# Performance work log

Measured on AMD Instinct MI355X. Metric: run time of the kernel, lower is better.

Reference implementation:

```python
import jax, jax.numpy as jnp
import numpy as np


def _ln(x, g, b, eps=1e-5):
    m = jnp.mean(x, axis=-1, keepdims=True)
    v = jnp.mean((x - m) ** 2, axis=-1, keepdims=True)
    return (x - m) * jax.lax.rsqrt(v + eps) * g + b


def _mlp2(x, w1, b1, w2, b2):
    # Linear -> SiLU -> Linear
    return jax.nn.silu(x @ w1 + b1) @ w2 + b2


def setup_inputs() -> dict:
    key = jax.random.key(0)
    ks = jax.random.split(key, 32)
    B, H, W = 1, 128, 256
    N = H * W                  # 32768 nodes
    K = 6
    E = N * K                  # 196608 edges
    Cin, Cout = 70, 69
    D, De, Hd, L = 256, 128, 512, 8
    s = 0.02

    def rn(k, shape):
        return jax.random.normal(k, shape, jnp.float32) * s

    inp = {
        "x": jax.random.normal(ks[0], (B, Cin, H, W), jnp.float32),
        "edge_index": jax.random.randint(ks[1], (2, E), 0, N, dtype=jnp.int32).astype(jnp.int64),
        "raw_edge_feat": jax.random.normal(ks[2], (E, 3), jnp.float32),
        # node encoder
        "enc_w1": rn(ks[3], (Cin, D)), "enc_b1": jnp.zeros((D,), jnp.float32),
        "enc_w2": rn(ks[4], (D, D)),   "enc_b2": jnp.zeros((D,), jnp.float32),
        # edge encoder
        "eenc_w1": rn(ks[5], (3, De)),  "eenc_b1": jnp.zeros((De,), jnp.float32),
        "eenc_w2": rn(ks[6], (De, De)), "eenc_b2": jnp.zeros((De,), jnp.float32),
        # processor (stacked over L layers)
        "pe_w1": rn(ks[7], (L, 2 * D + De, Hd)), "pe_b1": jnp.zeros((L, Hd), jnp.float32),
        "pe_w2": rn(ks[8], (L, Hd, De)),         "pe_b2": jnp.zeros((L, De), jnp.float32),
        "pe_g": jnp.ones((L, De), jnp.float32),  "pe_bt": jnp.zeros((L, De), jnp.float32),
        "pn_w1": rn(ks[9], (L, D + De, Hd)),     "pn_b1": jnp.zeros((L, Hd), jnp.float32),
        "pn_w2": rn(ks[10], (L, Hd, D)),         "pn_b2": jnp.zeros((L, D), jnp.float32),
        "pn_g": jnp.ones((L, D), jnp.float32),   "pn_bt": jnp.zeros((L, D), jnp.float32),
        # node decoder
        "dec_w1": rn(ks[11], (D, D)),   "dec_b1": jnp.zeros((D,), jnp.float32),
        "dec_w2": rn(ks[12], (D, Cout)), "dec_b2": jnp.zeros((Cout,), jnp.float32),
    }
    return inp


def reference(x, edge_index, raw_edge_feat,
              enc_w1, enc_b1, enc_w2, enc_b2,
              eenc_w1, eenc_b1, eenc_w2, eenc_b2,
              pe_w1, pe_b1, pe_w2, pe_b2, pe_g, pe_bt,
              pn_w1, pn_b1, pn_w2, pn_b2, pn_g, pn_bt,
              dec_w1, dec_b1, dec_w2, dec_b2):
    B, C, H, W = x.shape
    N = H * W
    src, dst = edge_index[0], edge_index[1]

    # encode: (B, N, Cin) -> (B, N, D)
    node = _mlp2(jnp.transpose(x.reshape(B, C, N), (0, 2, 1)), enc_w1, enc_b1, enc_w2, enc_b2)
    # edge encoder shared across batch, then broadcast to (B, E, De)
    edge = _mlp2(raw_edge_feat, eenc_w1, eenc_b1, eenc_w2, eenc_b2)
    edge = jnp.broadcast_to(edge[None], (B,) + edge.shape)

    def step(carry, p):
        node, edge = carry
        ew1, eb1, ew2, eb2, eg, ebt, nw1, nb1, nw2, nb2, ng, nbt = p
        # edge update: gather src/dst node feats, residual MLP + LayerNorm
        inp = jnp.concatenate([node[:, src], node[:, dst], edge], axis=-1)  # (B, E, 2D+De)
        edge = _ln(edge + _mlp2(inp, ew1, eb1, ew2, eb2), eg, ebt)
        # aggregate edges into destination nodes (scatter_add)
        agg = jax.vmap(lambda e: jax.ops.segment_sum(e, dst, num_segments=N))(edge)
        # node update: residual MLP + LayerNorm
        node = _ln(node + _mlp2(jnp.concatenate([node, agg], axis=-1), nw1, nb1, nw2, nb2), ng, nbt)
        return (node, edge), None

    (node, edge), _ = jax.lax.scan(
        step, (node, edge),
        (pe_w1, pe_b1, pe_w2, pe_b2, pe_g, pe_bt,
         pn_w1, pn_b1, pn_w2, pn_b2, pn_g, pn_bt))

    out = _mlp2(node, dec_w1, dec_b1, dec_w2, dec_b2)          # (B, N, Cout)
    return jnp.transpose(out, (0, 2, 1)).reshape(B, -1, H, W)   # (B, Cout, H, W)
```

## Files before the change

### kernel.cpp

```cpp
#include <hip/hip_runtime.h>


typedef __attribute__((ext_vector_type(8))) short bf16x8;
typedef __attribute__((ext_vector_type(4))) float f32x4;
typedef unsigned short u16;

#define NNODES 32768
#define NEDGES 196608

#define MFMA16(a, b, c) __builtin_amdgcn_mfma_f32_16x16x32_bf16((a), (b), (c), 0, 0, 0)

__device__ __forceinline__ u16 f2bf(float f) {
    unsigned u = __float_as_uint(f);
    unsigned r = (u + 0x7FFFu + ((u >> 16) & 1u)) >> 16;
    return (u16)r;
}
__device__ __forceinline__ float bf2f(u16 b) {
    return __uint_as_float(((unsigned)b) << 16);
}
__device__ __forceinline__ unsigned pack2(float a, float b) {
    return (unsigned)f2bf(a) | ((unsigned)f2bf(b) << 16);
}

__global__ void wtrans_kernel(const float* __restrict__ W, u16* __restrict__ WT,
                              int K, int Nout, int Kpad, int NP) {
    __shared__ u16 tile[32][33];
    const int k0 = blockIdx.x * 32, n0 = blockIdx.y * 32;
    const int tx = threadIdx.x & 31, ty = threadIdx.x >> 5;
    #pragma unroll
    for (int i = 0; i < 4; i++) {
        int k = k0 + ty + 8 * i, n = n0 + tx;
        float v = (k < K && n < Nout) ? W[(size_t)k * Nout + n] : 0.f;
        tile[ty + 8 * i][tx] = f2bf(v);
    }
    __syncthreads();
    #pragma unroll
    for (int i = 0; i < 4; i++) {
        int n = n0 + ty + 8 * i, k = k0 + tx;
        if (n < NP && k < Kpad) WT[(size_t)n * Kpad + k] = tile[tx][ty + 8 * i];
    }
}

__global__ void fragpack_kernel(const float* __restrict__ W, u16* __restrict__ F,
                                int K, int N, int CB, int NFRAG) {
    int b = blockIdx.z;
    int fr = blockIdx.x * 4 + (threadIdx.x >> 6);
    if (fr >= NFRAG) return;
    int l = threadIdx.x & 63;
    int ks = fr / CB, cb = fr % CB;
    int k0 = ks * 32 + ((l >> 4) * 8);
    int n = cb * 16 + (l & 15);
    u16 v[8];
    #pragma unroll
    for (int j = 0; j < 8; j++) {
        int k = k0 + j;
        float x = (k < K && n < N) ? W[((size_t)b * K + k) * N + n] : 0.f;
        v[j] = f2bf(x);
    }
    *(uint4*)(F + (((size_t)b * NFRAG + fr) * 64 + l) * 8) = *(const uint4*)v;
}

__global__ void idx_norm_kernel(const int* __restrict__ raw, int* __restrict__ sd) {
    __shared__ int nz;
    if (threadIdx.x == 0) nz = 0;
    __syncthreads();
    for (int i = threadIdx.x; i < 512; i += 256)
        if (raw[2 * i + 1] != 0) atomicAdd(&nz, 1);
    __syncthreads();
    const bool is64 = (nz == 0);
    int idx = blockIdx.x * 256 + threadIdx.x;
    if (idx < 2 * NEDGES) sd[idx] = is64 ? raw[2 * idx] : raw[idx];
}

__global__ void csr_count_kernel(const int* __restrict__ dsti, int* __restrict__ deg) {
    int e = blockIdx.x * 256 + threadIdx.x;
    atomicAdd(&deg[dsti[e]], 1);
}

__global__ void csr_scan_kernel(const int* __restrict__ deg, int* __restrict__ off,
                                int* __restrict__ cur) {
    __shared__ int part[1024];
    const int t = threadIdx.x;
    int local[32];
    int s = 0;
    #pragma unroll
    for (int i = 0; i < 32; i++) { local[i] = deg[t * 32 + i]; s += local[i]; }
    part[t] = s;
    __syncthreads();
    for (int d = 1; d < 1024; d <<= 1) {
        int v = (t >= d) ? part[t - d] : 0;
        __syncthreads();
        part[t] += v;
        __syncthreads();
    }
    int excl = (t == 0) ? 0 : part[t - 1];
    #pragma unroll
    for (int i = 0; i < 32; i++) {
        off[t * 32 + i] = excl;
        cur[t * 32 + i] = excl;
        excl += local[i];
    }
    if (t == 1023) off[NNODES] = excl;
}

__global__ void csr_fill_kernel(const int* __restrict__ dsti, int* __restrict__ cur,
                                int* __restrict__ perm) {
    int e = blockIdx.x * 256 + threadIdx.x;
    int pos = atomicAdd(&cur[dsti[e]], 1);
    perm[pos] = e;
}

__global__ void gather_kernel(const u16* __restrict__ edge_b, const int* __restrict__ perm,
                              const int* __restrict__ off, u16* __restrict__ aggB) {
    int idx = blockIdx.x * 256 + threadIdx.x;
    int n = idx >> 5, c = (idx & 31) * 4;
    int a = off[n], b = off[n + 1];
    float s0 = 0.f, s1 = 0.f, s2 = 0.f, s3 = 0.f;
    for (int i = a; i < b; i++) {
        uint2 v = *(const uint2*)(edge_b + (size_t)perm[i] * 128 + c);
        s0 += bf2f((u16)(v.x & 0xffff)); s1 += bf2f((u16)(v.x >> 16));
        s2 += bf2f((u16)(v.y & 0xffff)); s3 += bf2f((u16)(v.y >> 16));
    }
    uint2 o;
    o.x = pack2(s0, s1);
    o.y = pack2(s2, s3);
    *(uint2*)(aggB + (size_t)n * 128 + c) = o;
}

struct MlpP {
    const u16* A1;
    const u16* A1b;
    const float* Araw;
    const int* src;
    const int* dsti;
    const u16* W1F;
    const u16* W2F;
    const float* b1;
    const float* b2;
    const float* g;
    const float* bt;
    const float* resid;
    float* outF;
    u16* outB;
    float* outDec;
};

template <int K1, int NH, int NOUT, int IN, int OUT, int A1S>
__global__ __launch_bounds__(256, 2) void mlp_kernel(MlpP p) {
    static_assert(K1 % 32 == 0 && NH % 128 == 0, "dims");
    constexpr int KSTEPS = K1 / 32;
    constexpr int NT1 = NH / 64;
    constexpr int CB1 = NH / 16;
    constexpr int NFRAG2 = (NOUT + 15) / 16;
    constexpr int NT2 = (NFRAG2 + 3) / 4;
    constexpr int S2 = NH / 64;
    constexpr int SH2 = NH / 2 + 8;
    constexpr int SH_BYTES = 64 * SH2 * 2;
    constexpr int SMEM_I = (SH_BYTES > 8192 ? SH_BYTES : 8192);
    constexpr int SMEM = SMEM_I + 2560;

    __shared__ __align__(16) char smem[SMEM];
    u16* sA = (u16*)smem;
    u16* sH = (u16*)smem;
    float* sS1 = (float*)(smem + SMEM_I);
    float* sS2 = sS1 + 256;
    float* sMu = sS1 + 512;
    float* sRs = sS1 + 576;

    const int tid = threadIdx.x;
    const int wave = tid >> 6, lane = tid & 63;
    const int lhi = lane >> 4, llo = lane & 15;
    const int r0 = blockIdx.x * 64;
    const int key = (llo >> 1) & 3;

    const int sr = tid >> 2;
    const int sg = (tid & 3) ^ ((sr >> 1) & 3);
    int gsrc = 0, gdst = 0;
    if constexpr (IN == 0) { gsrc = p.src[r0 + sr]; gdst = p.dsti[r0 + sr]; }

    auto loadA = [&](int ks, uint4& d) {
        const int kb = ks * 32;
        if constexpr (IN == 0) {
            if (kb < 256)      d = *(const uint4*)(p.A1 + (size_t)gsrc * 256 + kb + sg * 8);
            else if (kb < 512) d = *(const uint4*)(p.A1 + (size_t)gdst * 256 + (kb - 256) + sg * 8);
            else               d = *(const uint4*)(p.A1b + (size_t)(r0 + sr) * 128 + (kb - 512) + sg * 8);
        } else if constexpr (IN == 1) {
            if (kb < 256) d = *(const uint4*)(p.A1 + (size_t)(r0 + sr) * 256 + kb + sg * 8);
            else          d = *(const uint4*)(p.A1b + (size_t)(r0 + sr) * 128 + (kb - 256) + sg * 8);
        } else if constexpr (IN == 2) {
            d = *(const uint4*)(p.A1 + (size_t)(r0 + sr) * A1S + kb + sg * 8);
        } else {
            uint4 v = {0u, 0u, 0u, 0u};
            if (sg == 0) {
                const float* q = p.Araw + (size_t)(r0 + sr) * 3;
                v.x = pack2(q[0], q[1]);
                v.y = pack2(q[2], 0.f);
            }
            d = v;
        }
    };
    auto loadB1 = [&](int ks, bf16x8 (&d)[NT1]) {
        #pragma unroll
        for (int j = 0; j < NT1; j++) {
            int cb = j * 4 + wave;
            d[j] = *(const bf16x8*)(p.W1F + ((size_t)(ks * CB1 + cb) * 64 + lane) * 8);
        }
    };

    const f32x4 fz = {0.f, 0.f, 0.f, 0.f};
    f32x4 acc[4][NT1];
    #pragma unroll
    for (int m = 0; m < 4; m++)
        #pragma unroll
        for (int j = 0; j < NT1; j++) acc[m][j] = fz;

    uint4 pa0, pa1, pa2;
    bf16x8 pb0[NT1], pb1[NT1];
    loadA(0, pa0);
    if constexpr (KSTEPS > 1) loadA(1, pa1);
    if constexpr (KSTEPS > 2) loadA(2, pa2);
    loadB1(0, pb0);
    if constexpr (KSTEPS > 1) loadB1(1, pb1);

    #pragma unroll
    for (int ks = 0; ks < KSTEPS; ks++) {
        uint4* sAw = (uint4*)(sA + (ks & 1) * 2048);
        sAw[tid] = (ks % 3 == 0) ? pa0 : (ks % 3 == 1) ? pa1 : pa2;
        if (ks + 3 < KSTEPS) {
            if (ks % 3 == 0) loadA(ks + 3, pa0);
            else if (ks % 3 == 1) loadA(ks + 3, pa1);
            else loadA(ks + 3, pa2);
        }
        __syncthreads();
        const u16* sAr = sA + (ks & 1) * 2048;
        bf16x8 a[4];
        #pragma unroll
        for (int m = 0; m < 4; m++)
            a[m] = *(const bf16x8*)(sAr + (m * 16 + llo) * 32 + (lhi ^ key) * 8);
        bf16x8 (&pbc)[NT1] = (ks & 1) ? pb1 : pb0;
        #pragma unroll
        for (int j = 0; j < NT1; j++)
            #pragma unroll
            for (int m = 0; m < 4; m++) acc[m][j] = MFMA16(a[m], pbc[j], acc[m][j]);
        if (ks + 2 < KSTEPS) loadB1(ks + 2, pbc);
    }
    __syncthreads();

    f32x4 acc2[4][NT2];
    #pragma unroll
    for (int m = 0; m < 4; m++)
        #pragma unroll
        for (int j = 0; j < NT2; j++) acc2[m][j] = fz;

    auto loadW2 = [&](int g, bf16x8 (&d)[NT2]) {
        #pragma unroll
        for (int j = 0; j < NT2; j++) {
            int f = j * 4 + wave;
            if (NFRAG2 % 4 == 0 || f < NFRAG2)
                d[j] = *(const bf16x8*)(p.W2F + ((size_t)(g * NFRAG2 + f) * 64 + lane) * 8);
        }
    };
    bf16x8 pw0[NT2], pw1[NT2];
    loadW2(0, pw0);
    loadW2(1, pw1);

    #pragma unroll
    for (int half = 0; half < 2; half++) {
        #pragma unroll
        for (int j = half * (NT1 / 2); j < (half + 1) * (NT1 / 2); j++) {
            int c = (j * 4 + wave) * 16 + llo;
            int coll = c - half * (NH / 2);
            float bias = p.b1[c];
            #pragma unroll
            for (int m = 0; m < 4; m++)
                #pragma unroll
                for (int r = 0; r < 4; r++) {
                    int row = m * 16 + lhi * 4 + r;
                    float v = acc[m][j][r] + bias;
                    float sgm = __builtin_amdgcn_rcpf(1.f + __expf(-v));
                    sH[row * SH2 + coll] = f2bf(v * sgm);
                }
        }
        __syncthreads();
        #pragma unroll
        for (int s = 0; s < S2; s++) {
            const int g = half * S2 + s;
            bf16x8 (&pwc)[NT2] = (g & 1) ? pw1 : pw0;
            bf16x8 a2[4];
            #pragma unroll
            for (int m = 0; m < 4; m++)
                a2[m] = *(const bf16x8*)(sH + (m * 16 + llo) * SH2 + s * 32 + lhi * 8);
            #pragma unroll
            for (int j = 0; j < NT2; j++)
                if (NFRAG2 % 4 == 0 || j * 4 + wave < NFRAG2)
                    #pragma unroll
                    for (int m = 0; m < 4; m++)
                        acc2[m][j] = MFMA16(a2[m], pwc[j], acc2[m][j]);
            if (g + 2 < 2 * S2) loadW2(g + 2, pwc);
        }
        __syncthreads();
    }

    if constexpr (OUT == 0) {
        float ps1[4][4], ps2[4][4];
        #pragma unroll
        for (int m = 0; m < 4; m++)
            #pragma unroll
            for (int r = 0; r < 4; r++) { ps1[m][r] = 0.f; ps2[m][r] = 0.f; }
        #pragma unroll
        for (int j = 0; j < NT2; j++) {
            int col = (j * 4 + wave) * 16 + llo;
            float bias = p.b2[col];
            #pragma unroll
            for (int m = 0; m < 4; m++)
                #pragma unroll
                for (int r = 0; r < 4; r++) {
                    int row = m * 16 + lhi * 4 + r;
                    float v = acc2[m][j][r] + bias + p.resid[(size_t)(r0 + row) * NOUT + col];
                    acc2[m][j][r] = v;
                    ps1[m][r] += v;
                    ps2[m][r] += v * v;
                }
        }
        #pragma unroll
        for (int mm = 1; mm < 16; mm <<= 1)
            #pragma unroll
            for (int m = 0; m < 4; m++)
                #pragma unroll
                for (int r = 0; r < 4; r++) {
                    ps1[m][r] += __shfl_xor(ps1[m][r], mm, 64);
                    ps2[m][r] += __shfl_xor(ps2[m][r], mm, 64);
                }
        if (llo == 0) {
            #pragma unroll
            for (int m = 0; m < 4; m++)
                #pragma unroll
                for (int r = 0; r < 4; r++) {
                    int row = m * 16 + lhi * 4 + r;
                    sS1[wave * 64 + row] = ps1[m][r];
                    sS2[wave * 64 + row] = ps2[m][r];
                }
        }
        __syncthreads();
        if (tid < 64) {
            float a = sS1[tid] + sS1[64 + tid] + sS1[128 + tid] + sS1[192 + tid];
            float b = sS2[tid] + sS2[64 + tid] + sS2[128 + tid] + sS2[192 + tid];
            float mu = a * (1.f / NOUT);
            float var = b * (1.f / NOUT) - mu * mu;
            sMu[tid] = mu;
            sRs[tid] = rsqrtf(var + 1e-5f);
        }
        __syncthreads();
        #pragma unroll
        for (int j = 0; j < NT2; j++) {
            int col = (j * 4 + wave) * 16 + llo;
            float gg = p.g[col], bb = p.bt[col];
            #pragma unroll
            for (int m = 0; m < 4; m++)
                #pragma unroll
                for (int r = 0; r < 4; r++) {
                    int row = m * 16 + lhi * 4 + r;
                    float v = (acc2[m][j][r] - sMu[row]) * sRs[row] * gg + bb;
                    size_t o = (size_t)(r0 + row) * NOUT + col;
                    p.outF[o] = v;
                    p.outB[o] = f2bf(v);
                }
        }
    } else if constexpr (OUT == 1) {
        #pragma unroll
        for (int j = 0; j < NT2; j++) {
            int col = (j * 4 + wave) * 16 + llo;
            float bias = p.b2[col];
            #pragma unroll
            for (int m = 0; m < 4; m++)
                #pragma unroll
                for (int r = 0; r < 4; r++) {
                    int row = m * 16 + lhi * 4 + r;
                    float v = acc2[m][j][r] + bias;
                    size_t o = (size_t)(r0 + row) * NOUT + col;
                    p.outF[o] = v;
                    p.outB[o] = f2bf(v);
                }
        }
    } else {
        #pragma unroll
        for (int j = 0; j < NT2; j++) {
            int f = j * 4 + wave;
            int col = f * 16 + llo;
            if (f < NFRAG2 && col < 69) {
                float bias = p.b2[col];
                #pragma unroll
                for (int m = 0; m < 4; m++)
                    #pragma unroll
                    for (int r = 0; r < 4; r++) {
                        int row = m * 16 + lhi * 4 + r;
                        p.outDec[(size_t)col * NNODES + (r0 + row)] = acc2[m][j][r] + bias;
                    }
            }
        }
    }
}

extern "C" void kernel_launch(void* const* d_in, const int* in_sizes, int n_in,
                              void* d_out, int out_size, void* d_ws, size_t ws_size,
                              hipStream_t stream) {
    (void)in_sizes; (void)n_in; (void)out_size; (void)ws_size;

    const float* x       = (const float*)d_in[0];
    const int*   eidx    = (const int*)d_in[1];
    const float* raw_e   = (const float*)d_in[2];
    const float* enc_w1  = (const float*)d_in[3];
    const float* enc_b1  = (const float*)d_in[4];
    const float* enc_w2  = (const float*)d_in[5];
    const float* enc_b2  = (const float*)d_in[6];
    const float* eenc_w1 = (const float*)d_in[7];
    const float* eenc_b1 = (const float*)d_in[8];
    const float* eenc_w2 = (const float*)d_in[9];
    const float* eenc_b2 = (const float*)d_in[10];
    const float* pe_w1   = (const float*)d_in[11];
    const float* pe_b1   = (const float*)d_in[12];
    const float* pe_w2   = (const float*)d_in[13];
    const float* pe_b2   = (const float*)d_in[14];
    const float* pe_g    = (const float*)d_in[15];
    const float* pe_bt   = (const float*)d_in[16];
    const float* pn_w1   = (const float*)d_in[17];
    const float* pn_b1   = (const float*)d_in[18];
    const float* pn_w2   = (const float*)d_in[19];
    const float* pn_b2   = (const float*)d_in[20];
    const float* pn_g    = (const float*)d_in[21];
    const float* pn_bt   = (const float*)d_in[22];
    const float* dec_w1  = (const float*)d_in[23];
    const float* dec_b1  = (const float*)d_in[24];
    const float* dec_w2  = (const float*)d_in[25];
    const float* dec_b2  = (const float*)d_in[26];

    char* ws = (char*)d_ws;
    size_t o = 0;
    auto alloc = [&](size_t bytes) -> void* {
        void* p = ws + o;
        o += (bytes + 255) & ~(size_t)255;
        return p;
    };
    float* node_f = (float*)alloc((size_t)NNODES * 256 * 4);
    u16*   node_b = (u16*)  alloc((size_t)NNODES * 256 * 2);
    float* edge_f = (float*)alloc((size_t)NEDGES * 128 * 4);
    u16*   edge_b = (u16*)  alloc((size_t)NEDGES * 128 * 2);
    u16*   aggB   = (u16*)  alloc((size_t)NNODES * 128 * 2);
    u16*   xT     = (u16*)  alloc((size_t)NNODES * 96 * 2);
    u16*   encw1F  = (u16*)alloc((size_t)96 * 256 * 2);
    u16*   encw2F  = (u16*)alloc((size_t)256 * 256 * 2);
    u16*   eencw1F = (u16*)alloc((size_t)32 * 128 * 2);
    u16*   eencw2F = (u16*)alloc((size_t)128 * 128 * 2);
    u16*   pew1F   = (u16*)alloc((size_t)8 * 640 * 512 * 2);
    u16*   pew2F   = (u16*)alloc((size_t)8 * 512 * 128 * 2);
    u16*   pnw1F   = (u16*)alloc((size_t)8 * 384 * 512 * 2);
    u16*   pnw2F   = (u16*)alloc((size_t)8 * 512 * 256 * 2);
    u16*   decw1F  = (u16*)alloc((size_t)256 * 256 * 2);
    u16*   decw2F  = (u16*)alloc((size_t)256 * 80 * 2);
    int*   sd     = (int*)  alloc((size_t)2 * NEDGES * 4);
    int*   deg    = (int*)  alloc((size_t)NNODES * 4);
    int*   off_   = (int*)  alloc((size_t)(NNODES + 1) * 4);
    int*   cur    = (int*)  alloc((size_t)NNODES * 4);
    int*   perm   = (int*)  alloc((size_t)NEDGES * 4);

    auto FP = [&](const float* W, u16* F, int K, int N, int KB, int CB, int batch) {
        int nf = KB * CB;
        dim3 g((nf + 3) / 4, 1, batch);
        fragpack_kernel<<<g, 256, 0, stream>>>(W, F, K, N, CB, nf);
    };
    FP(enc_w1,  encw1F,  70,  256, 3,  16, 1);
    FP(enc_w2,  encw2F,  256, 256, 8,  16, 1);
    FP(eenc_w1, eencw1F, 3,   128, 1,  8,  1);
    FP(eenc_w2, eencw2F, 128, 128, 4,  8,  1);
    FP(pe_w1,   pew1F,   640, 512, 20, 32, 8);
    FP(pe_w2,   pew2F,   512, 128, 16, 8,  8);
    FP(pn_w1,   pnw1F,   384, 512, 12, 32, 8);
    FP(pn_w2,   pnw2F,   512, 256, 16, 16, 8);
    FP(dec_w1,  decw1F,  256, 256, 8,  16, 1);
    FP(dec_w2,  decw2F,  256, 69,  8,  5,  1);
    {
        dim3 g(96 / 32, NNODES / 32, 1);
        wtrans_kernel<<<g, 256, 0, stream>>>(x, xT, 70, NNODES, 96, NNODES);
    }

    idx_norm_kernel<<<1536, 256, 0, stream>>>(eidx, sd);
    hipMemsetAsync(deg, 0, (size_t)NNODES * 4, stream);
    csr_count_kernel<<<NEDGES / 256, 256, 0, stream>>>(sd + NEDGES, deg);
    csr_scan_kernel<<<1, 1024, 0, stream>>>(deg, off_, cur);
    csr_fill_kernel<<<NEDGES / 256, 256, 0, stream>>>(sd + NEDGES, cur, perm);

    {
        MlpP p{};
        p.A1 = xT; p.W1F = encw1F; p.W2F = encw2F; p.b1 = enc_b1; p.b2 = enc_b2;
        p.outF = node_f; p.outB = node_b;
        mlp_kernel<96, 256, 256, 2, 1, 96><<<NNODES / 64, 256, 0, stream>>>(p);
    }
    {
        MlpP p{};
        p.Araw = raw_e; p.W1F = eencw1F; p.W2F = eencw2F; p.b1 = eenc_b1; p.b2 = eenc_b2;
        p.outF = edge_f; p.outB = edge_b;
        mlp_kernel<32, 128, 128, 3, 1, 0><<<NEDGES / 64, 256, 0, stream>>>(p);
    }

    for (int l = 0; l < 8; l++) {
        {
            MlpP p{};
            p.A1 = node_b; p.A1b = edge_b; p.src = sd; p.dsti = sd + NEDGES;
            p.W1F = pew1F + (size_t)l * 640 * 512;
            p.W2F = pew2F + (size_t)l * 512 * 128;
            p.b1 = pe_b1 + l * 512; p.b2 = pe_b2 + l * 128;
            p.g = pe_g + l * 128; p.bt = pe_bt + l * 128;
            p.resid = edge_f; p.outF = edge_f; p.outB = edge_b;
            mlp_kernel<640, 512, 128, 0, 0, 0><<<NEDGES / 64, 256, 0, stream>>>(p);
        }
        gather_kernel<<<NNODES * 32 / 256, 256, 0, stream>>>(edge_b, perm, off_, aggB);
        {
            MlpP p{};
            p.A1 = node_b; p.A1b = aggB;
            p.W1F = pnw1F + (size_t)l * 384 * 512;
            p.W2F = pnw2F + (size_t)l * 512 * 256;
            p.b1 = pn_b1 + l * 512; p.b2 = pn_b2 + l * 256;
            p.g = pn_g + l * 256; p.bt = pn_bt + l * 256;
            p.resid = node_f; p.outF = node_f; p.outB = node_b;
            mlp_kernel<384, 512, 256, 1, 0, 0><<<NNODES / 64, 256, 0, stream>>>(p);
        }
    }

    {
        MlpP p{};
        p.A1 = node_b; p.W1F = decw1F; p.W2F = decw2F; p.b1 = dec_b1; p.b2 = dec_b2;
        p.outDec = (float*)d_out;
        mlp_kernel<256, 256, 80, 2, 2, 256><<<NNODES / 64, 256, 0, stream>>>(p);
    }
}
```

Baseline: 2.265 ms.

## Store edges in dst-sorted order and load A fragments directly from global

Edges are permuted once into destination-sorted order: the edge encoder reads raw features through the permutation, and the per-layer edge MLP uses pre-sorted src/dst index arrays. The gather then reads contiguous edge rows without indirection. Separately, the first GEMM in the MLP kernel drops its LDS staging and barriers and loads A fragments straight from global memory into registers, prefetching one k-step ahead. This trades LDS traffic and syncs for uncoalesced 16-byte global loads and higher register pressure.

```diff
diff --git a/kernel.cpp b/kernel.cpp
--- a/kernel.cpp
+++ b/kernel.cpp
@@ -110,14 +110,22 @@
     perm[pos] = e;
 }
 
-__global__ void gather_kernel(const u16* __restrict__ edge_b, const int* __restrict__ perm,
+__global__ void esort_kernel(const int* __restrict__ sd, const int* __restrict__ perm,
+                             int* __restrict__ srcS, int* __restrict__ dstS) {
+    int i = blockIdx.x * 256 + threadIdx.x;
+    int e = perm[i];
+    srcS[i] = sd[e];
+    dstS[i] = sd[NEDGES + e];
+}
+
+__global__ void gather_kernel(const u16* __restrict__ edge_b,
                               const int* __restrict__ off, u16* __restrict__ aggB) {
     int idx = blockIdx.x * 256 + threadIdx.x;
     int n = idx >> 5, c = (idx & 31) * 4;
     int a = off[n], b = off[n + 1];
     float s0 = 0.f, s1 = 0.f, s2 = 0.f, s3 = 0.f;
     for (int i = a; i < b; i++) {
-        uint2 v = *(const uint2*)(edge_b + (size_t)perm[i] * 128 + c);
+        uint2 v = *(const uint2*)(edge_b + (size_t)i * 128 + c);
         s0 += bf2f((u16)(v.x & 0xffff)); s1 += bf2f((u16)(v.x >> 16));
         s2 += bf2f((u16)(v.y & 0xffff)); s3 += bf2f((u16)(v.y >> 16));
     }
@@ -155,12 +163,10 @@
     constexpr int NT2 = (NFRAG2 + 3) / 4;
     constexpr int S2 = NH / 64;
     constexpr int SH2 = NH / 2 + 8;
-    constexpr int SH_BYTES = 64 * SH2 * 2;
-    constexpr int SMEM_I = (SH_BYTES > 8192 ? SH_BYTES : 8192);
+    constexpr int SMEM_I = 64 * SH2 * 2;
     constexpr int SMEM = SMEM_I + 2560;
 
     __shared__ __align__(16) char smem[SMEM];
-    u16* sA = (u16*)smem;
     u16* sH = (u16*)smem;
     float* sS1 = (float*)(smem + SMEM_I);
     float* sS2 = sS1 + 256;
@@ -171,40 +177,65 @@
     const int wave = tid >> 6, lane = tid & 63;
     const int lhi = lane >> 4, llo = lane & 15;
     const int r0 = blockIdx.x * 64;
-    const int key = (llo >> 1) & 3;
-
-    const int sr = tid >> 2;
-    const int sg = (tid & 3) ^ ((sr >> 1) & 3);
-    int gsrc = 0, gdst = 0;
-    if constexpr (IN == 0) { gsrc = p.src[r0 + sr]; gdst = p.dsti[r0 + sr]; }
-
-    auto loadA = [&](int ks, uint4& d) {
+    const int ko = lhi * 8;
+
+    int rs[4], rd[4];
+    if constexpr (IN == 0) {
+        #pragma unroll
+        for (int m = 0; m < 4; m++) {
+            rs[m] = p.src[r0 + m * 16 + llo];
+            rd[m] = p.dsti[r0 + m * 16 + llo];
+        }
+    } else if constexpr (IN == 3) {
+        #pragma unroll
+        for (int m = 0; m < 4; m++) rs[m] = p.src[r0 + m * 16 + llo];
+    }
+
+    auto loadA4 = [&](int ks, bf16x8 (&d)[4]) {
         const int kb = ks * 32;
         if constexpr (IN == 0) {
-            if (kb < 256)      d = *(const uint4*)(p.A1 + (size_t)gsrc * 256 + kb + sg * 8);
-            else if (kb < 512) d = *(const uint4*)(p.A1 + (size_t)gdst * 256 + (kb - 256) + sg * 8);
-            else               d = *(const uint4*)(p.A1b + (size_t)(r0 + sr) * 128 + (kb - 512) + sg * 8);
+            if (kb < 256) {
+                #pragma unroll
+                for (int m = 0; m < 4; m++)
+                    d[m] = *(const bf16x8*)(p.A1 + (size_t)rs[m] * 256 + kb + ko);
+            } else if (kb < 512) {
+                #pragma unroll
+                for (int m = 0; m < 4; m++)
+                    d[m] = *(const bf16x8*)(p.A1 + (size_t)rd[m] * 256 + (kb - 256) + ko);
+            } else {
+                #pragma unroll
+                for (int m = 0; m < 4; m++)
+                    d[m] = *(const bf16x8*)(p.A1b + (size_t)(r0 + m * 16 + llo) * 128 + (kb - 512) + ko);
+            }
         } else if constexpr (IN == 1) {
-            if (kb < 256) d = *(const uint4*)(p.A1 + (size_t)(r0 + sr) * 256 + kb + sg * 8);
-            else          d = *(const uint4*)(p.A1b + (size_t)(r0 + sr) * 128 + (kb - 256) + sg * 8);
+            if (kb < 256) {
+                #pragma unroll
+                for (int m = 0; m < 4; m++)
+                    d[m] = *(const bf16x8*)(p.A1 + (size_t)(r0 + m * 16 + llo) * 256 + kb + ko);
+            } else {
+                #pragma unroll
+                for (int m = 0; m < 4; m++)
+                    d[m] = *(const bf16x8*)(p.A1b + (size_t)(r0 + m * 16 + llo) * 128 + (kb - 256) + ko);
+            }
         } else if constexpr (IN == 2) {
-            d = *(const uint4*)(p.A1 + (size_t)(r0 + sr) * A1S + kb + sg * 8);
+            #pragma unroll
+            for (int m = 0; m < 4; m++)
+                d[m] = *(const bf16x8*)(p.A1 + (size_t)(r0 + m * 16 + llo) * A1S + kb + ko);
         } else {
-            uint4 v = {0u, 0u, 0u, 0u};
-            if (sg == 0) {
-                const float* q = p.Araw + (size_t)(r0 + sr) * 3;
-                v.x = pack2(q[0], q[1]);
-                v.y = pack2(q[2], 0.f);
+            #pragma unroll
+            for (int m = 0; m < 4; m++) {
+                u16 v[8] = {0, 0, 0, 0, 0, 0, 0, 0};
+                if (lhi == 0) {
+                    const float* q = p.Araw + (size_t)rs[m] * 3;
+                    v[0] = f2bf(q[0]); v[1] = f2bf(q[1]); v[2] = f2bf(q[2]);
+                }
+                d[m] = *(const bf16x8*)v;
             }
-            d = v;
         }
     };
-    auto loadB1 = [&](int ks, bf16x8 (&d)[NT1]) {
-        #pragma unroll
-        for (int j = 0; j < NT1; j++) {
-            int cb = j * 4 + wave;
-            d[j] = *(const bf16x8*)(p.W1F + ((size_t)(ks * CB1 + cb) * 64 + lane) * 8);
-        }
+    auto loadB1frag = [&](int ks, int j) -> bf16x8 {
+        int cb = j * 4 + wave;
+        return *(const bf16x8*)(p.W1F + ((size_t)(ks * CB1 + cb) * 64 + lane) * 8);
     };
 
     const f32x4 fz = {0.f, 0.f, 0.f, 0.f};
@@ -214,37 +245,24 @@
         #pragma unroll
         for (int j = 0; j < NT1; j++) acc[m][j] = fz;
 
-    uint4 pa0, pa1, pa2;
-    bf16x8 pb0[NT1], pb1[NT1];
-    loadA(0, pa0);
-    if constexpr (KSTEPS > 1) loadA(1, pa1);
-    if constexpr (KSTEPS > 2) loadA(2, pa2);
-    loadB1(0, pb0);
-    if constexpr (KSTEPS > 1) loadB1(1, pb1);
+    bf16x8 paA[4], paB[4];
+    bf16x8 pb[NT1];
+    loadA4(0, paA);
+    #pragma unroll
+    for (int j = 0; j < NT1; j++) pb[j] = loadB1frag(0, j);
 
     #pragma unroll
     for (int ks = 0; ks < KSTEPS; ks++) {
-        uint4* sAw = (uint4*)(sA + (ks & 1) * 2048);
-        sAw[tid] = (ks % 3 == 0) ? pa0 : (ks % 3 == 1) ? pa1 : pa2;
-        if (ks + 3 < KSTEPS) {
-            if (ks % 3 == 0) loadA(ks + 3, pa0);
-            else if (ks % 3 == 1) loadA(ks + 3, pa1);
-            else loadA(ks + 3, pa2);
-        }
-        __syncthreads();
-        const u16* sAr = sA + (ks & 1) * 2048;
-        bf16x8 a[4];
-        #pragma unroll
-        for (int m = 0; m < 4; m++)
-            a[m] = *(const bf16x8*)(sAr + (m * 16 + llo) * 32 + (lhi ^ key) * 8);
-        bf16x8 (&pbc)[NT1] = (ks & 1) ? pb1 : pb0;
-        #pragma unroll
-        for (int j = 0; j < NT1; j++)
-            #pragma unroll
-            for (int m = 0; m < 4; m++) acc[m][j] = MFMA16(a[m], pbc[j], acc[m][j]);
-        if (ks + 2 < KSTEPS) loadB1(ks + 2, pbc);
-    }
-    __syncthreads();
+        bf16x8 (&cur)[4] = (ks & 1) ? paB : paA;
+        bf16x8 (&nxt)[4] = (ks & 1) ? paA : paB;
+        if (ks + 1 < KSTEPS) loadA4(ks + 1, nxt);
+        #pragma unroll
+        for (int j = 0; j < NT1; j++) {
+            #pragma unroll
+            for (int m = 0; m < 4; m++) acc[m][j] = MFMA16(cur[m], pb[j], acc[m][j]);
+            if (ks + 1 < KSTEPS) pb[j] = loadB1frag(ks + 1, j);
+        }
+    }
 
     f32x4 acc2[4][NT2];
     #pragma unroll
@@ -462,6 +480,8 @@
     int*   off_   = (int*)  alloc((size_t)(NNODES + 1) * 4);
     int*   cur    = (int*)  alloc((size_t)NNODES * 4);
     int*   perm   = (int*)  alloc((size_t)NEDGES * 4);
+    int*   srcS   = (int*)  alloc((size_t)NEDGES * 4);
+    int*   dstS   = (int*)  alloc((size_t)NEDGES * 4);
 
     auto FP = [&](const float* W, u16* F, int K, int N, int KB, int CB, int batch) {
         int nf = KB * CB;
@@ -488,6 +508,7 @@
     csr_count_kernel<<<NEDGES / 256, 256, 0, stream>>>(sd + NEDGES, deg);
     csr_scan_kernel<<<1, 1024, 0, stream>>>(deg, off_, cur);
     csr_fill_kernel<<<NEDGES / 256, 256, 0, stream>>>(sd + NEDGES, cur, perm);
+    esort_kernel<<<NEDGES / 256, 256, 0, stream>>>(sd, perm, srcS, dstS);
 
     {
         MlpP p{};
@@ -497,7 +518,8 @@
     }
     {
         MlpP p{};
-        p.Araw = raw_e; p.W1F = eencw1F; p.W2F = eencw2F; p.b1 = eenc_b1; p.b2 = eenc_b2;
+        p.Araw = raw_e; p.src = perm;
+        p.W1F = eencw1F; p.W2F = eencw2F; p.b1 = eenc_b1; p.b2 = eenc_b2;
         p.outF = edge_f; p.outB = edge_b;
         mlp_kernel<32, 128, 128, 3, 1, 0><<<NEDGES / 64, 256, 0, stream>>>(p);
     }
@@ -505,7 +527,7 @@
     for (int l = 0; l < 8; l++) {
         {
             MlpP p{};
-            p.A1 = node_b; p.A1b = edge_b; p.src = sd; p.dsti = sd + NEDGES;
+            p.A1 = node_b; p.A1b = edge_b; p.src = srcS; p.dsti = dstS;
             p.W1F = pew1F + (size_t)l * 640 * 512;
             p.W2F = pew2F + (size_t)l * 512 * 128;
             p.b1 = pe_b1 + l * 512; p.b2 = pe_b2 + l * 128;
@@ -513,7 +535,7 @@
             p.resid = edge_f; p.outF = edge_f; p.outB = edge_b;
             mlp_kernel<640, 512, 128, 0, 0, 0><<<NEDGES / 64, 256, 0, stream>>>(p);
         }
-        gather_kernel<<<NNODES * 32 / 256, 256, 0, stream>>>(edge_b, perm, off_, aggB);
+        gather_kernel<<<NNODES * 32 / 256, 256, 0, stream>>>(edge_b, off_, aggB);
         {
             MlpP p{};
             p.A1 = node_b; p.A1b = aggB;
```

Measured after the change: 3.613 ms. 1.6x slower.

## Store edges in destination-sorted order and drop fp32 residual copies

Applied to the files above, without the earlier changes.

Permutes edges into CSR (destination-sorted) order once up front, so the edge encoder reads raw features through perm and each layer's edge MLP uses sorted src/dst indices. The gather then reads contiguous edge rows instead of indirect rows through perm. The fp32 node and edge state buffers are also removed: residuals are read from and written to the bf16 copies only. This cuts memory traffic but lowers residual precision to bf16 across the 8 layers, which may reduce accuracy.

```diff
diff --git a/kernel.cpp b/kernel.cpp
--- a/kernel.cpp
+++ b/kernel.cpp
@@ -110,14 +110,22 @@
     perm[pos] = e;
 }
 
-__global__ void gather_kernel(const u16* __restrict__ edge_b, const int* __restrict__ perm,
+__global__ void esort_kernel(const int* __restrict__ sd, const int* __restrict__ perm,
+                             int* __restrict__ srcS, int* __restrict__ dstS) {
+    int i = blockIdx.x * 256 + threadIdx.x;
+    int e = perm[i];
+    srcS[i] = sd[e];
+    dstS[i] = sd[NEDGES + e];
+}
+
+__global__ void gather_kernel(const u16* __restrict__ edge_b,
                               const int* __restrict__ off, u16* __restrict__ aggB) {
     int idx = blockIdx.x * 256 + threadIdx.x;
     int n = idx >> 5, c = (idx & 31) * 4;
     int a = off[n], b = off[n + 1];
     float s0 = 0.f, s1 = 0.f, s2 = 0.f, s3 = 0.f;
     for (int i = a; i < b; i++) {
-        uint2 v = *(const uint2*)(edge_b + (size_t)perm[i] * 128 + c);
+        uint2 v = *(const uint2*)(edge_b + (size_t)i * 128 + c);
         s0 += bf2f((u16)(v.x & 0xffff)); s1 += bf2f((u16)(v.x >> 16));
         s2 += bf2f((u16)(v.y & 0xffff)); s3 += bf2f((u16)(v.y >> 16));
     }
@@ -139,8 +147,7 @@
     const float* b2;
     const float* g;
     const float* bt;
-    const float* resid;
-    float* outF;
+    const u16* residB;
     u16* outB;
     float* outDec;
 };
@@ -177,6 +184,7 @@
     const int sg = (tid & 3) ^ ((sr >> 1) & 3);
     int gsrc = 0, gdst = 0;
     if constexpr (IN == 0) { gsrc = p.src[r0 + sr]; gdst = p.dsti[r0 + sr]; }
+    if constexpr (IN == 3) { gsrc = p.src[r0 + sr]; }
 
     auto loadA = [&](int ks, uint4& d) {
         const int kb = ks * 32;
@@ -192,7 +200,7 @@
         } else {
             uint4 v = {0u, 0u, 0u, 0u};
             if (sg == 0) {
-                const float* q = p.Araw + (size_t)(r0 + sr) * 3;
+                const float* q = p.Araw + (size_t)gsrc * 3;
                 v.x = pack2(q[0], q[1]);
                 v.y = pack2(q[2], 0.f);
             }
@@ -316,7 +324,8 @@
                 #pragma unroll
                 for (int r = 0; r < 4; r++) {
                     int row = m * 16 + lhi * 4 + r;
-                    float v = acc2[m][j][r] + bias + p.resid[(size_t)(r0 + row) * NOUT + col];
+                    float v = acc2[m][j][r] + bias +
+                              bf2f(p.residB[(size_t)(r0 + row) * NOUT + col]);
                     acc2[m][j][r] = v;
                     ps1[m][r] += v;
                     ps2[m][r] += v * v;
@@ -361,9 +370,7 @@
                 for (int r = 0; r < 4; r++) {
                     int row = m * 16 + lhi * 4 + r;
                     float v = (acc2[m][j][r] - sMu[row]) * sRs[row] * gg + bb;
-                    size_t o = (size_t)(r0 + row) * NOUT + col;
-                    p.outF[o] = v;
-                    p.outB[o] = f2bf(v);
+                    p.outB[(size_t)(r0 + row) * NOUT + col] = f2bf(v);
                 }
         }
     } else if constexpr (OUT == 1) {
@@ -377,9 +384,7 @@
                 for (int r = 0; r < 4; r++) {
                     int row = m * 16 + lhi * 4 + r;
                     float v = acc2[m][j][r] + bias;
-                    size_t o = (size_t)(r0 + row) * NOUT + col;
-                    p.outF[o] = v;
-                    p.outB[o] = f2bf(v);
+                    p.outB[(size_t)(r0 + row) * NOUT + col] = f2bf(v);
                 }
         }
     } else {
@@ -441,9 +446,7 @@
         o += (bytes + 255) & ~(size_t)255;
         return p;
     };
-    float* node_f = (float*)alloc((size_t)NNODES * 256 * 4);
     u16*   node_b = (u16*)  alloc((size_t)NNODES * 256 * 2);
-    float* edge_f = (float*)alloc((size_t)NEDGES * 128 * 4);
     u16*   edge_b = (u16*)  alloc((size_t)NEDGES * 128 * 2);
     u16*   aggB   = (u16*)  alloc((size_t)NNODES * 128 * 2);
     u16*   xT     = (u16*)  alloc((size_t)NNODES * 96 * 2);
@@ -462,6 +465,8 @@
     int*   off_   = (int*)  alloc((size_t)(NNODES + 1) * 4);
     int*   cur    = (int*)  alloc((size_t)NNODES * 4);
     int*   perm   = (int*)  alloc((size_t)NEDGES * 4);
+    int*   srcS   = (int*)  alloc((size_t)NEDGES * 4);
+    int*   dstS   = (int*)  alloc((size_t)NEDGES * 4);
 
     auto FP = [&](const float* W, u16* F, int K, int N, int KB, int CB, int batch) {
         int nf = KB * CB;
@@ -488,32 +493,34 @@
     csr_count_kernel<<<NEDGES / 256, 256, 0, stream>>>(sd + NEDGES, deg);
     csr_scan_kernel<<<1, 1024, 0, stream>>>(deg, off_, cur);
     csr_fill_kernel<<<NEDGES / 256, 256, 0, stream>>>(sd + NEDGES, cur, perm);
+    esort_kernel<<<NEDGES / 256, 256, 0, stream>>>(sd, perm, srcS, dstS);
 
     {
         MlpP p{};
         p.A1 = xT; p.W1F = encw1F; p.W2F = encw2F; p.b1 = enc_b1; p.b2 = enc_b2;
-        p.outF = node_f; p.outB = node_b;
+        p.outB = node_b;
         mlp_kernel<96, 256, 256, 2, 1, 96><<<NNODES / 64, 256, 0, stream>>>(p);
     }
     {
         MlpP p{};
-        p.Araw = raw_e; p.W1F = eencw1F; p.W2F = eencw2F; p.b1 = eenc_b1; p.b2 = eenc_b2;
-        p.outF = edge_f; p.outB = edge_b;
+        p.Araw = raw_e; p.src = perm;
+        p.W1F = eencw1F; p.W2F = eencw2F; p.b1 = eenc_b1; p.b2 = eenc_b2;
+        p.outB = edge_b;
         mlp_kernel<32, 128, 128, 3, 1, 0><<<NEDGES / 64, 256, 0, stream>>>(p);
     }
 
     for (int l = 0; l < 8; l++) {
         {
             MlpP p{};
-            p.A1 = node_b; p.A1b = edge_b; p.src = sd; p.dsti = sd + NEDGES;
+            p.A1 = node_b; p.A1b = edge_b; p.src = srcS; p.dsti = dstS;
             p.W1F = pew1F + (size_t)l * 640 * 512;
             p.W2F = pew2F + (size_t)l * 512 * 128;
             p.b1 = pe_b1 + l * 512; p.b2 = pe_b2 + l * 128;
             p.g = pe_g + l * 128; p.bt = pe_bt + l * 128;
-            p.resid = edge_f; p.outF = edge_f; p.outB = edge_b;
+            p.residB = edge_b; p.outB = edge_b;
             mlp_kernel<640, 512, 128, 0, 0, 0><<<NEDGES / 64, 256, 0, stream>>>(p);
         }
-        gather_kernel<<<NNODES * 32 / 256, 256, 0, stream>>>(edge_b, perm, off_, aggB);
+        gather_kernel<<<NNODES * 32 / 256, 256, 0, stream>>>(edge_b, off_, aggB);
         {
             MlpP p{};
             p.A1 = node_b; p.A1b = aggB;
@@ -521,7 +528,7 @@
             p.W2F = pnw2F + (size_t)l * 512 * 256;
             p.b1 = pn_b1 + l * 512; p.b2 = pn_b2 + l * 256;
             p.g = pn_g + l * 256; p.bt = pn_bt + l * 256;
-            p.resid = node_f; p.outF = node_f; p.outB = node_b;
+            p.residB = node_b; p.outB = node_b;
             mlp_kernel<384, 512, 256, 1, 0, 0><<<NNODES / 64, 256, 0, stream>>>(p);
         }
     }
```

New measurement: 2.043 ms. 9.8% less time.
